# Kernel tuning notes

Measured on AMD Instinct MI355X. Metric: run time of the kernel, lower is better.

The kernel has to match this reference:

```python
import jax, jax.numpy as jnp
import numpy as np


def setup_inputs() -> dict:
    key = jax.random.key(0)
    k1, k2 = jax.random.split(key)
    inputs = jax.random.normal(k1, (32, 4096, 64), dtype=jnp.float32)
    embed = jax.random.normal(k2, (64, 1024), dtype=jnp.float32)  # [embed_dim, n_embed]
    return {"inputs": inputs, "embed": embed}


def reference(inputs, embed):
    # Eval-mode forward of VectorQuantizer (self.training == False, no EMA update).
    embed_dim, n_embed = embed.shape
    flat = inputs.reshape(-1, embed_dim)  # [N, D]
    # distances[n, k] = ||flat_n||^2 - 2 flat_n . e_k + ||e_k||^2
    distances = (
        jnp.sum(flat * flat, axis=1, keepdims=True)
        - 2.0 * (flat @ embed)
        + jnp.sum(embed * embed, axis=0, keepdims=True)
    )  # [N, n_embed]
    # torch.argmax(-distances, 1) == argmin(distances, 1) (same first-occurrence tie-break)
    encoding_indices = jnp.argmin(distances, axis=1)  # [N] int
    idx = encoding_indices.reshape(inputs.shape[:-1])  # [B, T]
    # quantize: F.embedding(idx, embed.T) -> gather rows of embed.T
    quantized = jnp.take(embed.T, idx, axis=0)  # [B, T, D]
    codes = jnp.concatenate([inputs, quantized], axis=-1)  # [B, T, 2D]
    # straight-through estimator
    quantized_st = inputs + jax.lax.stop_gradient(quantized - inputs)
    return quantized_st, codes, idx
```

## Files before the change

kernel.cpp:

```cpp
#include <hip/hip_runtime.h>

#define D 64
#define KCODES 1024
#define PTS_PER_BLK 256
#define MTILES 16
#define NT 16
#define WL_CAP 8192

typedef short bf16x8 __attribute__((ext_vector_type(8)));
typedef float f32x4 __attribute__((ext_vector_type(4)));

static __device__ __forceinline__ short f2bf(float f) {
  unsigned u = __float_as_uint(f);
  u += 0x7FFF + ((u >> 16) & 1);
  return (short)(u >> 16);
}

static __device__ __forceinline__ void evalExact(const float* __restrict__ inputs,
                                                 const float* __restrict__ embedT,
                                                 const float* __restrict__ en2,
                                                 const float* s_fn2,
                                                 int p0blk, int pl, int c,
                                                 unsigned long long* s_best) {
  int p = p0blk + pl;
  const float* f = inputs + (size_t)p * D;
  const float* e = embedT + (size_t)c * D;
  float a0 = 0.f, a1 = 0.f, a2 = 0.f, a3 = 0.f;
#pragma unroll
  for (int d = 0; d < D; d += 4) {
    a0 = fmaf(f[d + 0], e[d + 0], a0);
    a1 = fmaf(f[d + 1], e[d + 1], a1);
    a2 = fmaf(f[d + 2], e[d + 2], a2);
    a3 = fmaf(f[d + 3], e[d + 3], a3);
  }
  float dot = (a0 + a1) + (a2 + a3);
  float dist = fmaf(-2.f, dot, s_fn2[pl]) + en2[c];
  unsigned long long key = ((unsigned long long)__float_as_uint(dist) << 32) | (unsigned)c;
  atomicMin(&s_best[pl], key);
}

__global__ void __launch_bounds__(256) vq_prep_codes(const float* __restrict__ embed,
                                                     float* __restrict__ embedT,
                                                     unsigned short* __restrict__ embedTb,
                                                     float* __restrict__ en2,
                                                     int* __restrict__ en2max_bits) {
  int k = blockIdx.x * 256 + threadIdx.x;
  float row[D];
  float s = 0.f;
#pragma unroll
  for (int d = 0; d < D; ++d) {
    float e = embed[d * KCODES + k];
    row[d] = e;
    s = fmaf(e, e, s);
  }
  en2[k] = s;
  float4* o4 = reinterpret_cast<float4*>(embedT + (size_t)k * D);
#pragma unroll
  for (int j = 0; j < 16; ++j)
    o4[j] = make_float4(row[4 * j], row[4 * j + 1], row[4 * j + 2], row[4 * j + 3]);
  unsigned us[32];
#pragma unroll
  for (int j = 0; j < 32; ++j) {
    unsigned lo = (unsigned short)f2bf(row[2 * j]);
    unsigned hi = (unsigned short)f2bf(row[2 * j + 1]);
    us[j] = lo | (hi << 16);
  }
  uint4* ob = reinterpret_cast<uint4*>(embedTb + (size_t)k * D);
#pragma unroll
  for (int j = 0; j < 8; ++j) ob[j] = make_uint4(us[4 * j], us[4 * j + 1], us[4 * j + 2], us[4 * j + 3]);
  float m = s;
#pragma unroll
  for (int off = 32; off; off >>= 1) m = fmaxf(m, __shfl_down(m, off, 64));
  if ((threadIdx.x & 63) == 0) atomicMax(en2max_bits, __float_as_int(m));
}

__global__ void __launch_bounds__(256, 2) vq_main_kernel(
    const float* __restrict__ inputs, const float* __restrict__ embedT,
    const unsigned short* __restrict__ embedTb, const float* __restrict__ en2,
    const int* __restrict__ en2max_bits,
    float* __restrict__ out_q, float* __restrict__ out_codes,
    float* __restrict__ out_idx) {
  __shared__ unsigned long long s_best[PTS_PER_BLK];
  __shared__ unsigned s_wl[WL_CAP];
  __shared__ int s_wcount;
  __shared__ float s_fn2[PTS_PER_BLK];

  const int tid = threadIdx.x;
  const int w = tid >> 6;
  const int l = tid & 63;
  const int l15 = l & 15;
  const int lg = l >> 4;
  const int p0blk = blockIdx.x * PTS_PER_BLK;
  const int cbase = w * 256;

  s_best[tid] = ~0ull;
  if (tid == 0) s_wcount = 0;

  {
    const float4* i4 = reinterpret_cast<const float4*>(inputs + (size_t)(p0blk + tid) * D);
    float s = 0.f;
#pragma unroll
    for (int j = 0; j < 16; ++j) {
      float4 v = i4[j];
      s = fmaf(v.x, v.x, s); s = fmaf(v.y, v.y, s);
      s = fmaf(v.z, v.z, s); s = fmaf(v.w, v.w, s);
    }
    s_fn2[tid] = s;
  }

  const float en2max = __int_as_float(*en2max_bits);

  bf16x8 bfr[NT][2];
#pragma unroll
  for (int t = 0; t < NT; ++t) {
    const bf16x8* bp = reinterpret_cast<const bf16x8*>(
        embedTb + (size_t)(cbase + 16 * t + l15) * D + lg * 8);
    bfr[t][0] = bp[0];
    bfr[t][1] = bp[4];
  }
  float en2v[NT];
#pragma unroll
  for (int t = 0; t < NT; ++t) en2v[t] = en2[cbase + 16 * t + l15];

  __syncthreads();

  float4 A0, A1, A2, A3;
  {
    const float* arow = inputs + (size_t)(p0blk + l15) * D + lg * 8;
    A0 = *reinterpret_cast<const float4*>(arow + 0);
    A1 = *reinterpret_cast<const float4*>(arow + 4);
    A2 = *reinterpret_cast<const float4*>(arow + 32);
    A3 = *reinterpret_cast<const float4*>(arow + 36);
  }

#pragma unroll 1
  for (int mt = 0; mt < MTILES; ++mt) {
    const int mtn = (mt + 1 < MTILES) ? mt + 1 : mt;
    const float* an = inputs + (size_t)(p0blk + mtn * 16 + l15) * D + lg * 8;
    float4 N0 = *reinterpret_cast<const float4*>(an + 0);
    float4 N1 = *reinterpret_cast<const float4*>(an + 4);
    float4 N2 = *reinterpret_cast<const float4*>(an + 32);
    float4 N3 = *reinterpret_cast<const float4*>(an + 36);

    bf16x8 af0, af1;
    af0[0] = f2bf(A0.x); af0[1] = f2bf(A0.y); af0[2] = f2bf(A0.z); af0[3] = f2bf(A0.w);
    af0[4] = f2bf(A1.x); af0[5] = f2bf(A1.y); af0[6] = f2bf(A1.z); af0[7] = f2bf(A1.w);
    af1[0] = f2bf(A2.x); af1[1] = f2bf(A2.y); af1[2] = f2bf(A2.z); af1[3] = f2bf(A2.w);
    af1[4] = f2bf(A3.x); af1[5] = f2bf(A3.y); af1[6] = f2bf(A3.z); af1[7] = f2bf(A3.w);

    f32x4 acc[NT];
#pragma unroll
    for (int t = 0; t < NT; ++t) acc[t] = (f32x4){0.f, 0.f, 0.f, 0.f};
#pragma unroll
    for (int t = 0; t < NT; ++t)
      acc[t] = __builtin_amdgcn_mfma_f32_16x16x32_bf16(af0, bfr[t][0], acc[t], 0, 0, 0);
#pragma unroll
    for (int t = 0; t < NT; ++t)
      acc[t] = __builtin_amdgcn_mfma_f32_16x16x32_bf16(af1, bfr[t][1], acc[t], 0, 0, 0);

    float fnv[4];
#pragma unroll
    for (int r = 0; r < 4; ++r) fnv[r] = s_fn2[mt * 16 + lg * 4 + r];
#pragma unroll
    for (int t = 0; t < NT; ++t)
#pragma unroll
      for (int r = 0; r < 4; ++r)
        acc[t][r] = fmaf(-2.f, acc[t][r], fnv[r]) + en2v[t];

    float thr[4];
#pragma unroll
    for (int r = 0; r < 4; ++r) {
      float mm = acc[0][r];
#pragma unroll
      for (int t = 1; t < NT; ++t) mm = fminf(mm, acc[t][r]);
#pragma unroll
      for (int s = 1; s < 16; s <<= 1) mm = fminf(mm, __shfl_xor(mm, s, 16));
      thr[r] = mm + (0.03125f * sqrtf(fnv[r] * en2max) + 0.01f);
    }
#pragma unroll
    for (int t = 0; t < NT; ++t)
#pragma unroll
      for (int r = 0; r < 4; ++r)
        if (acc[t][r] <= thr[r]) {
          int pl = mt * 16 + lg * 4 + r;
          int c = cbase + 16 * t + l15;
          int pos = atomicAdd(&s_wcount, 1);
          if (pos < WL_CAP) s_wl[pos] = (unsigned)((pl << 10) | c);
          else evalExact(inputs, embedT, en2, s_fn2, p0blk, pl, c, s_best);
        }

    A0 = N0; A1 = N1; A2 = N2; A3 = N3;
  }

  __syncthreads();

  int wc = s_wcount; if (wc > WL_CAP) wc = WL_CAP;
  for (int i = tid; i < wc; i += 256)
    evalExact(inputs, embedT, en2, s_fn2, p0blk, (int)(s_wl[i] >> 10), (int)(s_wl[i] & 1023), s_best);
  __syncthreads();

  const int sub = tid & 3;
#pragma unroll 1
  for (int pass = 0; pass < 4; ++pass) {
    int pl = pass * 64 + (tid >> 2);
    unsigned long long key = s_best[pl];
    int c = (int)(unsigned)(key & 0xFFFFFFFFu);
    int p = p0blk + pl;
    const f32x4* qrow = reinterpret_cast<const f32x4*>(embedT + (size_t)c * D);
    const f32x4* frow = reinterpret_cast<const f32x4*>(inputs + (size_t)p * D);
    f32x4* oq = reinterpret_cast<f32x4*>(out_q + (size_t)p * D);
    f32x4* oc = reinterpret_cast<f32x4*>(out_codes + (size_t)p * 2 * D);
#pragma unroll
    for (int j = 0; j < 4; ++j) {
      int i4 = j * 4 + sub;
      f32x4 qv = qrow[i4];
      f32x4 fv = frow[i4];
      __builtin_nontemporal_store(qv, &oq[i4]);
      __builtin_nontemporal_store(fv, &oc[i4]);
      __builtin_nontemporal_store(qv, &oc[16 + i4]);
    }
    if (sub == 0) __builtin_nontemporal_store((float)c, &out_idx[p]);
  }
}

extern "C" void kernel_launch(void* const* d_in, const int* in_sizes, int n_in,
                              void* d_out, int out_size, void* d_ws, size_t ws_size,
                              hipStream_t stream) {
  const float* inputs = (const float*)d_in[0];
  const float* embed  = (const float*)d_in[1];
  int N = in_sizes[0] / D;

  float* embedT          = (float*)d_ws;
  unsigned short* embedTb = (unsigned short*)(embedT + KCODES * D);
  float* en2             = (float*)(embedTb + KCODES * D);
  float* fn2_unused      = en2 + KCODES;
  int* en2max_bits       = (int*)(fn2_unused + N);

  float* out = (float*)d_out;
  float* out_q     = out;
  float* out_codes = out + (size_t)N * D;
  float* out_idx   = out + (size_t)N * D * 3;

  vq_prep_codes<<<KCODES / 256, 256, 0, stream>>>(embed, embedT, embedTb, en2, en2max_bits);
  vq_main_kernel<<<N / PTS_PER_BLK, 256, 0, stream>>>(inputs, embedT, embedTb, en2,
                                                      en2max_bits, out_q, out_codes, out_idx);
}
```

Before: 314.2 us.

## Halve points per block, chunk codebook B fragments, and fuse input copy into codes

Reduces points per block from 256 to 128 and splits each wave's 256-code slice into two 128-code chunks, so only eight B fragments live in registers at a time. Launch bounds rise to four blocks per SM for higher occupancy. The inputs half of the codes output is now written during the norm pass instead of being re-read in the epilogue, and nontemporal stores become plain stores. In exchange, the A tile is reloaded and reconverted once per chunk, software prefetch of the next A tile is dropped, and the grid has twice as many blocks.

```diff
diff --git a/kernel.cpp b/kernel.cpp
--- a/kernel.cpp
+++ b/kernel.cpp
@@ -2,10 +2,11 @@
 
 #define D 64
 #define KCODES 1024
-#define PTS_PER_BLK 256
-#define MTILES 16
-#define NT 16
-#define WL_CAP 8192
+#define PTS_PER_BLK 128
+#define MTILES 8
+#define NT 8
+#define NCHUNK 2
+#define WL_CAP 4096
 
 typedef short bf16x8 __attribute__((ext_vector_type(8)));
 typedef float f32x4 __attribute__((ext_vector_type(4)));
@@ -74,7 +75,7 @@
   if ((threadIdx.x & 63) == 0) atomicMax(en2max_bits, __float_as_int(m));
 }
 
-__global__ void __launch_bounds__(256, 2) vq_main_kernel(
+__global__ void __launch_bounds__(256, 4) vq_main_kernel(
     const float* __restrict__ inputs, const float* __restrict__ embedT,
     const unsigned short* __restrict__ embedTb, const float* __restrict__ en2,
     const int* __restrict__ en2max_bits,
@@ -91,17 +92,19 @@
   const int l15 = l & 15;
   const int lg = l >> 4;
   const int p0blk = blockIdx.x * PTS_PER_BLK;
-  const int cbase = w * 256;
-
-  s_best[tid] = ~0ull;
+
+  if (tid < PTS_PER_BLK) s_best[tid] = ~0ull;
   if (tid == 0) s_wcount = 0;
 
-  {
-    const float4* i4 = reinterpret_cast<const float4*>(inputs + (size_t)(p0blk + tid) * D);
+  if (tid < PTS_PER_BLK) {
+    const int p = p0blk + tid;
+    const float4* i4 = reinterpret_cast<const float4*>(inputs + (size_t)p * D);
+    float4* oc0 = reinterpret_cast<float4*>(out_codes + (size_t)p * 2 * D);
     float s = 0.f;
 #pragma unroll
     for (int j = 0; j < 16; ++j) {
       float4 v = i4[j];
+      oc0[j] = v;
       s = fmaf(v.x, v.x, s); s = fmaf(v.y, v.y, s);
       s = fmaf(v.z, v.z, s); s = fmaf(v.w, v.w, s);
     }
@@ -110,86 +113,78 @@
 
   const float en2max = __int_as_float(*en2max_bits);
 
-  bf16x8 bfr[NT][2];
-#pragma unroll
-  for (int t = 0; t < NT; ++t) {
-    const bf16x8* bp = reinterpret_cast<const bf16x8*>(
-        embedTb + (size_t)(cbase + 16 * t + l15) * D + lg * 8);
-    bfr[t][0] = bp[0];
-    bfr[t][1] = bp[4];
-  }
-  float en2v[NT];
-#pragma unroll
-  for (int t = 0; t < NT; ++t) en2v[t] = en2[cbase + 16 * t + l15];
-
   __syncthreads();
 
-  float4 A0, A1, A2, A3;
-  {
-    const float* arow = inputs + (size_t)(p0blk + l15) * D + lg * 8;
-    A0 = *reinterpret_cast<const float4*>(arow + 0);
-    A1 = *reinterpret_cast<const float4*>(arow + 4);
-    A2 = *reinterpret_cast<const float4*>(arow + 32);
-    A3 = *reinterpret_cast<const float4*>(arow + 36);
-  }
-
 #pragma unroll 1
-  for (int mt = 0; mt < MTILES; ++mt) {
-    const int mtn = (mt + 1 < MTILES) ? mt + 1 : mt;
-    const float* an = inputs + (size_t)(p0blk + mtn * 16 + l15) * D + lg * 8;
-    float4 N0 = *reinterpret_cast<const float4*>(an + 0);
-    float4 N1 = *reinterpret_cast<const float4*>(an + 4);
-    float4 N2 = *reinterpret_cast<const float4*>(an + 32);
-    float4 N3 = *reinterpret_cast<const float4*>(an + 36);
-
-    bf16x8 af0, af1;
-    af0[0] = f2bf(A0.x); af0[1] = f2bf(A0.y); af0[2] = f2bf(A0.z); af0[3] = f2bf(A0.w);
-    af0[4] = f2bf(A1.x); af0[5] = f2bf(A1.y); af0[6] = f2bf(A1.z); af0[7] = f2bf(A1.w);
-    af1[0] = f2bf(A2.x); af1[1] = f2bf(A2.y); af1[2] = f2bf(A2.z); af1[3] = f2bf(A2.w);
-    af1[4] = f2bf(A3.x); af1[5] = f2bf(A3.y); af1[6] = f2bf(A3.z); af1[7] = f2bf(A3.w);
-
-    f32x4 acc[NT];
-#pragma unroll
-    for (int t = 0; t < NT; ++t) acc[t] = (f32x4){0.f, 0.f, 0.f, 0.f};
-#pragma unroll
-    for (int t = 0; t < NT; ++t)
-      acc[t] = __builtin_amdgcn_mfma_f32_16x16x32_bf16(af0, bfr[t][0], acc[t], 0, 0, 0);
-#pragma unroll
-    for (int t = 0; t < NT; ++t)
-      acc[t] = __builtin_amdgcn_mfma_f32_16x16x32_bf16(af1, bfr[t][1], acc[t], 0, 0, 0);
-
-    float fnv[4];
-#pragma unroll
-    for (int r = 0; r < 4; ++r) fnv[r] = s_fn2[mt * 16 + lg * 4 + r];
-#pragma unroll
-    for (int t = 0; t < NT; ++t)
-#pragma unroll
-      for (int r = 0; r < 4; ++r)
-        acc[t][r] = fmaf(-2.f, acc[t][r], fnv[r]) + en2v[t];
-
-    float thr[4];
-#pragma unroll
-    for (int r = 0; r < 4; ++r) {
-      float mm = acc[0][r];
-#pragma unroll
-      for (int t = 1; t < NT; ++t) mm = fminf(mm, acc[t][r]);
-#pragma unroll
-      for (int s = 1; s < 16; s <<= 1) mm = fminf(mm, __shfl_xor(mm, s, 16));
-      thr[r] = mm + (0.03125f * sqrtf(fnv[r] * en2max) + 0.01f);
-    }
-#pragma unroll
-    for (int t = 0; t < NT; ++t)
-#pragma unroll
-      for (int r = 0; r < 4; ++r)
-        if (acc[t][r] <= thr[r]) {
-          int pl = mt * 16 + lg * 4 + r;
-          int c = cbase + 16 * t + l15;
-          int pos = atomicAdd(&s_wcount, 1);
-          if (pos < WL_CAP) s_wl[pos] = (unsigned)((pl << 10) | c);
-          else evalExact(inputs, embedT, en2, s_fn2, p0blk, pl, c, s_best);
-        }
-
-    A0 = N0; A1 = N1; A2 = N2; A3 = N3;
+  for (int ch = 0; ch < NCHUNK; ++ch) {
+    const int cb = w * 256 + ch * 128;
+
+    bf16x8 bfr[NT][2];
+    float en2v[NT];
+#pragma unroll
+    for (int t = 0; t < NT; ++t) {
+      const bf16x8* bp = reinterpret_cast<const bf16x8*>(
+          embedTb + (size_t)(cb + 16 * t + l15) * D + lg * 8);
+      bfr[t][0] = bp[0];
+      bfr[t][1] = bp[4];
+      en2v[t] = en2[cb + 16 * t + l15];
+    }
+
+#pragma unroll 1
+    for (int mt = 0; mt < MTILES; ++mt) {
+      const int p0 = p0blk + mt * 16;
+      const float* arow = inputs + (size_t)(p0 + l15) * D + lg * 8;
+      float4 a0 = *reinterpret_cast<const float4*>(arow + 0);
+      float4 a1 = *reinterpret_cast<const float4*>(arow + 4);
+      float4 a2 = *reinterpret_cast<const float4*>(arow + 32);
+      float4 a3 = *reinterpret_cast<const float4*>(arow + 36);
+      bf16x8 af0, af1;
+      af0[0] = f2bf(a0.x); af0[1] = f2bf(a0.y); af0[2] = f2bf(a0.z); af0[3] = f2bf(a0.w);
+      af0[4] = f2bf(a1.x); af0[5] = f2bf(a1.y); af0[6] = f2bf(a1.z); af0[7] = f2bf(a1.w);
+      af1[0] = f2bf(a2.x); af1[1] = f2bf(a2.y); af1[2] = f2bf(a2.z); af1[3] = f2bf(a2.w);
+      af1[4] = f2bf(a3.x); af1[5] = f2bf(a3.y); af1[6] = f2bf(a3.z); af1[7] = f2bf(a3.w);
+
+      f32x4 acc[NT];
+#pragma unroll
+      for (int t = 0; t < NT; ++t) acc[t] = (f32x4){0.f, 0.f, 0.f, 0.f};
+#pragma unroll
+      for (int t = 0; t < NT; ++t)
+        acc[t] = __builtin_amdgcn_mfma_f32_16x16x32_bf16(af0, bfr[t][0], acc[t], 0, 0, 0);
+#pragma unroll
+      for (int t = 0; t < NT; ++t)
+        acc[t] = __builtin_amdgcn_mfma_f32_16x16x32_bf16(af1, bfr[t][1], acc[t], 0, 0, 0);
+
+      float fnv[4];
+#pragma unroll
+      for (int r = 0; r < 4; ++r) fnv[r] = s_fn2[mt * 16 + lg * 4 + r];
+#pragma unroll
+      for (int t = 0; t < NT; ++t)
+#pragma unroll
+        for (int r = 0; r < 4; ++r)
+          acc[t][r] = fmaf(-2.f, acc[t][r], fnv[r]) + en2v[t];
+
+      float thr[4];
+#pragma unroll
+      for (int r = 0; r < 4; ++r) {
+        float mm = acc[0][r];
+#pragma unroll
+        for (int t = 1; t < NT; ++t) mm = fminf(mm, acc[t][r]);
+#pragma unroll
+        for (int s = 1; s < 16; s <<= 1) mm = fminf(mm, __shfl_xor(mm, s, 16));
+        thr[r] = mm + (0.03125f * sqrtf(fnv[r] * en2max) + 0.01f);
+      }
+#pragma unroll
+      for (int t = 0; t < NT; ++t)
+#pragma unroll
+        for (int r = 0; r < 4; ++r)
+          if (acc[t][r] <= thr[r]) {
+            int pl = mt * 16 + lg * 4 + r;
+            int c = cb + 16 * t + l15;
+            int pos = atomicAdd(&s_wcount, 1);
+            if (pos < WL_CAP) s_wl[pos] = (unsigned)((pl << 10) | c);
+            else evalExact(inputs, embedT, en2, s_fn2, p0blk, pl, c, s_best);
+          }
+    }
   }
 
   __syncthreads();
@@ -201,25 +196,22 @@
 
   const int sub = tid & 3;
 #pragma unroll 1
-  for (int pass = 0; pass < 4; ++pass) {
+  for (int pass = 0; pass < 2; ++pass) {
     int pl = pass * 64 + (tid >> 2);
     unsigned long long key = s_best[pl];
     int c = (int)(unsigned)(key & 0xFFFFFFFFu);
     int p = p0blk + pl;
     const f32x4* qrow = reinterpret_cast<const f32x4*>(embedT + (size_t)c * D);
-    const f32x4* frow = reinterpret_cast<const f32x4*>(inputs + (size_t)p * D);
     f32x4* oq = reinterpret_cast<f32x4*>(out_q + (size_t)p * D);
     f32x4* oc = reinterpret_cast<f32x4*>(out_codes + (size_t)p * 2 * D);
 #pragma unroll
     for (int j = 0; j < 4; ++j) {
       int i4 = j * 4 + sub;
       f32x4 qv = qrow[i4];
-      f32x4 fv = frow[i4];
-      __builtin_nontemporal_store(qv, &oq[i4]);
-      __builtin_nontemporal_store(fv, &oc[i4]);
-      __builtin_nontemporal_store(qv, &oc[16 + i4]);
-    }
-    if (sub == 0) __builtin_nontemporal_store((float)c, &out_idx[p]);
+      oq[i4] = qv;
+      oc[16 + i4] = qv;
+    }
+    if (sub == 0) out_idx[p] = (float)c;
   }
 }
 
```

Measured after the change: 413.6 us. 1.32x slower.
